# Performance work log

Measured on AMD Instinct MI355X. Metric: run time of the kernel, lower is better.

## Reference

```python
import jax, jax.numpy as jnp
import numpy as np

N = 100000      # nodes
E = 1600000     # edges (before self-loops)
IN = 128        # in_channels
H = 8           # heads (layer 0)
C = 8           # hidden_node_channels_per_head
OUT = 64        # out_channels (layer 1, single head, concat=False)
NEG_SLOPE = 0.2 # PyG GATConv LeakyReLU slope


def setup_inputs() -> dict:
    key = jax.random.key(0)
    ks = jax.random.split(key, 10)
    x = jax.random.normal(ks[0], (N, IN), jnp.float32)
    edge_index = jax.random.randint(ks[1], (2, E), 0, N, dtype=jnp.int32)
    s0 = 1.0 / np.sqrt(IN)
    s1 = 1.0 / np.sqrt(H * C)
    return {
        "x": x,
        "edge_index": edge_index,
        "W0": jax.random.normal(ks[2], (IN, H * C), jnp.float32) * s0,
        "att_src0": jax.random.normal(ks[3], (H, C), jnp.float32) * s1,
        "att_dst0": jax.random.normal(ks[4], (H, C), jnp.float32) * s1,
        "b0": jnp.zeros((H * C,), jnp.float32),
        "W1": jax.random.normal(ks[5], (H * C, OUT), jnp.float32) * s1,
        "att_src1": jax.random.normal(ks[6], (1, OUT), jnp.float32) * s1,
        "att_dst1": jax.random.normal(ks[7], (1, OUT), jnp.float32) * s1,
        "b1": jnp.zeros((OUT,), jnp.float32),
    }


def _gat_conv(x, src, dst, W, a_src, a_dst, b, heads, ch, concat):
    # x: [N, F_in]; src/dst: [E'] (self-loops included)
    xW = (x @ W).reshape(N, heads, ch)                     # [N, H, C]
    a_s = jnp.einsum('nhc,hc->nh', xW, a_src)              # [N, H]
    a_d = jnp.einsum('nhc,hc->nh', xW, a_dst)              # [N, H]
    e = jax.nn.leaky_relu(a_s[src] + a_d[dst], NEG_SLOPE)  # [E', H]
    # segment softmax over incoming edges of each dst node
    m = jax.ops.segment_max(e, dst, num_segments=N)        # [N, H]
    ex = jnp.exp(e - m[dst])
    denom = jax.ops.segment_sum(ex, dst, num_segments=N)   # [N, H]
    alpha = ex / denom[dst]                                # [E', H]
    out = jax.ops.segment_sum(alpha[:, :, None] * xW[src], dst, num_segments=N)  # [N, H, C]
    if concat:
        return out.reshape(N, heads * ch) + b
    return out.mean(axis=1) + b


def reference(x, edge_index, W0, att_src0, att_dst0, b0, W1, att_src1, att_dst1, b1):
    src, dst = edge_index[0], edge_index[1]
    loops = jnp.arange(N, dtype=src.dtype)                 # PyG add_self_loops=True
    src = jnp.concatenate([src, loops])
    dst = jnp.concatenate([dst, loops])
    # layer 0: GATConv(IN -> C per head, H heads, concat) ; ELU (dropout = identity at eval)
    h = jax.nn.elu(_gat_conv(x, src, dst, W0, att_src0, att_dst0, b0, H, C, True))
    # layer 1: GATConv(H*C -> OUT, 1 head, concat=False) ; ELU
    out = jax.nn.elu(_gat_conv(h, src, dst, W1, att_src1, att_dst1, b1, 1, OUT, False))
    return out
```

## Files before the change

### kernel.cpp

```cpp
#include <hip/hip_runtime.h>
#include <hip/hip_fp16.h>
#include <math.h>


#define CAPS 16
#define STRIDE 17
#define NBMAX 512
#define LOG2E 1.44269504f

typedef _Float16 h2_t  __attribute__((ext_vector_type(2)));
typedef _Float16 h8_t  __attribute__((ext_vector_type(8)));
typedef float    f4_t  __attribute__((ext_vector_type(4)));
typedef unsigned int u4_t __attribute__((ext_vector_type(4)));

__device__ __forceinline__ float lrelu(float v) { return v >= 0.f ? v : 0.2f * v; }
__device__ __forceinline__ float eluf(float v)  { return v > 0.f ? v : expm1f(v); }

#define MIX_LO(acc, pk, w) asm("v_fma_mix_f32 %0, %1, %2, %0 op_sel:[0,0,0] op_sel_hi:[1,0,0]" : "+v"(acc) : "v"(pk), "v"(w))
#define MIX_HI(acc, pk, w) asm("v_fma_mix_f32 %0, %1, %2, %0 op_sel:[1,0,0] op_sel_hi:[1,0,0]" : "+v"(acc) : "v"(pk), "v"(w))

__global__ void kPrep(const float* __restrict__ W0,
                      const float* __restrict__ aS0, const float* __restrict__ aD0,
                      const float* __restrict__ W1,
                      __half* __restrict__ W0swz, __half* __restrict__ W1swz)
{
    for (int g = threadIdx.x; g < 1280; g += 256) {
        int col  = g & 15;
        int quad = (g >> 4) & 3;
        int ks   = (g >> 6) & 3;
        int ct   = g >> 8;
        #pragma unroll
        for (int j = 0; j < 8; j++) {
            int k = ks * 32 + quad * 8 + j;
            float v;
            if (ct < 4) {
                v = W0[k * 64 + ct * 16 + col];
            } else {
                int h = col & 7;
                const float* att = (col < 8) ? aS0 : aD0;
                v = 0.f;
                #pragma unroll
                for (int cc = 0; cc < 8; cc++)
                    v += W0[k * 64 + h * 8 + cc] * att[h * 8 + cc];
            }
            W0swz[g * 8 + j] = __float2half(v);
        }
    }
    for (int g = threadIdx.x; g < 512; g += 256) {
        int col  = g & 15;
        int quad = (g >> 4) & 3;
        int ks   = (g >> 6) & 1;
        int ct   = g >> 7;
        #pragma unroll
        for (int j = 0; j < 8; j++) {
            int k = ks * 32 + quad * 8 + j;
            W1swz[g * 8 + j] = __float2half(W1[k * 64 + ct * 16 + col]);
        }
    }
}

__device__ __forceinline__ void gemm_body(
    int gb, const float* __restrict__ x, int N,
    __half* __restrict__ xw, float* __restrict__ as, float* __restrict__ ad,
    h8_t* Bl)
{
    int wave = threadIdx.x >> 6, lane = threadIdx.x & 63;
    int row0 = gb * 128 + wave * 16;
    if (row0 >= N) return;
    int quad = lane >> 4, c16 = lane & 15;
    int myrow = min(row0 + c16, N - 1);
    const float* xr = x + (size_t)myrow * 128;
    h8_t a[4];
    #pragma unroll
    for (int ks = 0; ks < 4; ks++) {
        int kb = ks * 32 + quad * 8;
        float4 v0 = *(const float4*)(xr + kb);
        float4 v1 = *(const float4*)(xr + kb + 4);
        h8_t av;
        av[0] = (_Float16)v0.x; av[1] = (_Float16)v0.y;
        av[2] = (_Float16)v0.z; av[3] = (_Float16)v0.w;
        av[4] = (_Float16)v1.x; av[5] = (_Float16)v1.y;
        av[6] = (_Float16)v1.z; av[7] = (_Float16)v1.w;
        a[ks] = av;
    }
    int rbase = row0 + quad * 4;
    #pragma unroll
    for (int ct = 0; ct < 5; ct++) {
        f4_t acc = {0.f, 0.f, 0.f, 0.f};
        #pragma unroll
        for (int ks = 0; ks < 4; ks++) {
            h8_t b = Bl[(ct * 4 + ks) * 64 + lane];
            acc = __builtin_amdgcn_mfma_f32_16x16x32_f16(a[ks], b, acc, 0, 0, 0);
        }
        if (ct < 4) {
            int col = ct * 16 + c16;
            #pragma unroll
            for (int r = 0; r < 4; r++) {
                int row = rbase + r;
                if (row < N) xw[(size_t)row * 64 + col] = __float2half(acc[r]);
            }
        } else {
            #pragma unroll
            for (int r = 0; r < 4; r++) {
                int row = rbase + r;
                if (row < N) {
                    float sc = acc[r] * LOG2E;
                    if (c16 < 8) as[(size_t)row * 8 + c16] = sc;
                    else         ad[(size_t)row * 8 + (c16 - 8)] = sc;
                }
            }
        }
    }
}

__global__ __launch_bounds__(512, 4) void kGB(
    const float* __restrict__ x, const __half* __restrict__ W0swz, int N,
    __half* __restrict__ xw, float* __restrict__ as, float* __restrict__ ad,
    int gemmBlocks,
    const int* __restrict__ src, const int* __restrict__ dst, int E, int perBlock,
    unsigned* __restrict__ bucketBuf, int* __restrict__ gcur, int NB, int cap,
    int binBlocks)
{
    __shared__ __align__(16) char smem[NBMAX * STRIDE * 4 + NBMAX * 4];
    int b = blockIdx.x;
    int T = gemmBlocks + binBlocks;
    int lo = (int)((long long)b * gemmBlocks / T);
    int hi = (int)((long long)(b + 1) * gemmBlocks / T);
    if (hi > lo) {
        h8_t* Bl = (h8_t*)smem;
        const float4* s = (const float4*)W0swz;
        float4* d = (float4*)smem;
        for (int i = threadIdx.x; i < 1280; i += 512) d[i] = s[i];
        __syncthreads();
        gemm_body(lo, x, N, xw, as, ad, Bl);
    } else {
        int pb = b - hi;
        unsigned* stage = (unsigned*)smem;
        int* scnt = (int*)(smem + NBMAX * STRIDE * 4);
        int tid = threadIdx.x;
        for (int i = tid; i < NB; i += 512) scnt[i] = 0;
        __syncthreads();
        int e0 = pb * perBlock, e1 = min(E, e0 + perBlock);
        for (int i = e0 + tid; i < e1; i += 512) {
            int d2 = dst[i], s2 = src[i];
            int bk = d2 >> 8;
            unsigned rec = ((unsigned)(d2 & 255) << 22) | (unsigned)s2;
            int pos = atomicAdd(&scnt[bk], 1);
            if (pos < CAPS) {
                stage[bk * STRIDE + pos] = rec;
            } else {
                int g = atomicAdd(&gcur[bk], 1);
                if (g < cap) bucketBuf[(size_t)bk * cap + g] = rec;
            }
        }
        __syncthreads();
        for (int t = tid; t < NB; t += 512) {
            int n = min(scnt[t], CAPS);
            if (n > 0) {
                int gb2 = atomicAdd(&gcur[t], n);
                unsigned* gp = &bucketBuf[(size_t)t * cap + gb2];
                for (int j = 0; j < n; j++)
                    if (gb2 + j < cap) gp[j] = stage[t * STRIDE + j];
            }
        }
    }
}

__global__ __launch_bounds__(256) void kP2(
    const unsigned* __restrict__ bucketBuf, const int* __restrict__ gcur,
    int NB, int cap, int N, int* __restrict__ row, int* __restrict__ adj)
{
    __shared__ int deg[256];
    __shared__ int curl[256];
    __shared__ int sc[256];
    int b = blockIdx.x, tid = threadIdx.x;
    int lo = b << 8;
    int hi = min(N, lo + 256);
    int cnt = hi - lo;
    int size = min(gcur[b], cap);
    int part = 0;
    for (int i = tid; i < b; i += 256) part += min(gcur[i], cap);
    sc[tid] = part;
    __syncthreads();
    for (int off = 128; off > 0; off >>= 1) {
        if (tid < off) sc[tid] += sc[tid + off];
        __syncthreads();
    }
    int bbase = sc[0];
    __syncthreads();
    deg[tid] = 0;
    __syncthreads();
    const unsigned* buf = bucketBuf + (size_t)b * cap;
    for (int e = tid; e < size; e += 256) atomicAdd(&deg[buf[e] >> 22], 1);
    __syncthreads();
    int d = deg[tid];
    sc[tid] = d;
    __syncthreads();
    for (int off = 1; off < 256; off <<= 1) {
        int xv = (tid >= off) ? sc[tid - off] : 0;
        __syncthreads();
        sc[tid] += xv;
        __syncthreads();
    }
    int o = (tid ? sc[tid - 1] : 0);
    curl[tid] = o;
    if (tid < cnt) row[lo + tid] = bbase + o;
    if (b == NB - 1 && tid == 0) row[N] = bbase + size;
    __syncthreads();
    for (int e = tid; e < size; e += 256) {
        unsigned r = buf[e];
        int l = r >> 22;
        int p = atomicAdd(&curl[l], 1);
        adj[bbase + p] = (int)(r & 0x3FFFFF);
    }
}

__global__ __launch_bounds__(256) void k_agg8(
    const __half* __restrict__ xw, const float* __restrict__ as, const float* __restrict__ ad,
    const int* __restrict__ row, const int* __restrict__ adj,
    const float* __restrict__ bias, int N, __half* __restrict__ hbuf)
{
    int n = (blockIdx.x * 256 + threadIdx.x) >> 5;
    int lane = threadIdx.x & 63;
    int sub  = lane & 31;
    if (n >= N) return;
    int e4 = sub >> 3;
    int hh = sub & 7;
    int rs = row[n], re = row[n + 1];
    const u4_t* xwv = (const u4_t*)xw;
    float adv = ad[(unsigned)n * 8u + hh];
    float shift = lrelu(as[(unsigned)n * 8u + hh] + adv);
    float accv[8];
    #pragma unroll
    for (int k = 0; k < 8; k++) accv[k] = 0.f;
    float dsum = 0.f;

    int j = rs;
    bool vA0 = j + e4 < re,      vB0 = j + 4 + e4 < re;
    int  sA0 = adj[(unsigned)(vA0 ? j + e4 : 0)];
    int  sB0 = adj[(unsigned)(vB0 ? j + 4 + e4 : 0)];
    bool vA1 = j + 8 + e4 < re,  vB1 = j + 12 + e4 < re;
    int  sA1 = adj[(unsigned)(vA1 ? j + 8 + e4 : 0)];
    int  sB1 = adj[(unsigned)(vB1 ? j + 12 + e4 : 0)];
    float eA0 = lrelu(as[(unsigned)sA0 * 8u + hh] + adv);
    float eB0 = lrelu(as[(unsigned)sB0 * 8u + hh] + adv);
    u4_t xA0 = xwv[(unsigned)sA0 * 8u + hh];
    u4_t xB0 = xwv[(unsigned)sB0 * 8u + hh];
    float eA1, eB1; u4_t xA1, xB1;

    for (;;) {
        {
            bool vA2 = j + 16 + e4 < re, vB2 = j + 20 + e4 < re;
            int nsA = adj[(unsigned)(vA2 ? j + 16 + e4 : 0)];
            int nsB = adj[(unsigned)(vB2 ? j + 20 + e4 : 0)];
            eA1 = lrelu(as[(unsigned)sA1 * 8u + hh] + adv);
            eB1 = lrelu(as[(unsigned)sB1 * 8u + hh] + adv);
            xA1 = xwv[(unsigned)sA1 * 8u + hh];
            xB1 = xwv[(unsigned)sB1 * 8u + hh];
            float wA = vA0 ? __builtin_amdgcn_exp2f(eA0 - shift) : 0.f;
            float wB = vB0 ? __builtin_amdgcn_exp2f(eB0 - shift) : 0.f;
            dsum += wA + wB;
            #pragma unroll
            for (int q = 0; q < 4; q++) {
                MIX_LO(accv[2 * q],     xA0[q], wA);
                MIX_HI(accv[2 * q + 1], xA0[q], wA);
            }
            #pragma unroll
            for (int q = 0; q < 4; q++) {
                MIX_LO(accv[2 * q],     xB0[q], wB);
                MIX_HI(accv[2 * q + 1], xB0[q], wB);
            }
            vA0 = vA2; vB0 = vB2; sA0 = nsA; sB0 = nsB;
        }
        j += 8;
        if (!__any(vA1)) break;
        {
            bool vA2 = j + 16 + e4 < re, vB2 = j + 20 + e4 < re;
            int nsA = adj[(unsigned)(vA2 ? j + 16 + e4 : 0)];
            int nsB = adj[(unsigned)(vB2 ? j + 20 + e4 : 0)];
            eA0 = lrelu(as[(unsigned)sA0 * 8u + hh] + adv);
            eB0 = lrelu(as[(unsigned)sB0 * 8u + hh] + adv);
            xA0 = xwv[(unsigned)sA0 * 8u + hh];
            xB0 = xwv[(unsigned)sB0 * 8u + hh];
            float wA = vA1 ? __builtin_amdgcn_exp2f(eA1 - shift) : 0.f;
            float wB = vB1 ? __builtin_amdgcn_exp2f(eB1 - shift) : 0.f;
            dsum += wA + wB;
            #pragma unroll
            for (int q = 0; q < 4; q++) {
                MIX_LO(accv[2 * q],     xA1[q], wA);
                MIX_HI(accv[2 * q + 1], xA1[q], wA);
            }
            #pragma unroll
            for (int q = 0; q < 4; q++) {
                MIX_LO(accv[2 * q],     xB1[q], wB);
                MIX_HI(accv[2 * q + 1], xB1[q], wB);
            }
            vA1 = vA2; vB1 = vB2; sA1 = nsA; sB1 = nsB;
        }
        j += 8;
        if (!__any(vA0)) break;
    }
    #pragma unroll
    for (int k = 0; k < 8; k++) {
        accv[k] += __shfl_xor(accv[k], 8, 64);
        accv[k] += __shfl_xor(accv[k], 16, 64);
    }
    dsum += __shfl_xor(dsum, 8, 64);
    dsum += __shfl_xor(dsum, 16, 64);
    if (e4 == 0) {
        float inv = 1.f / (1.f + dsum);
        h8_t sv = *(const h8_t*)(xw + (size_t)n * 64 + hh * 8);
        float4 b0 = *(const float4*)(bias + hh * 8);
        float4 b1 = *(const float4*)(bias + hh * 8 + 4);
        float bb[8] = {b0.x, b0.y, b0.z, b0.w, b1.x, b1.y, b1.z, b1.w};
        h8_t o;
        #pragma unroll
        for (int k = 0; k < 8; k++) {
            float v = (accv[k] + (float)sv[k]) * inv + bb[k];
            o[k] = (_Float16)eluf(v);
        }
        *(h8_t*)(hbuf + (size_t)n * 64 + hh * 8) = o;
    }
}

__global__ __launch_bounds__(512, 4) void kTF1(
    const __half* __restrict__ h, const __half* __restrict__ W1swz,
    const float* __restrict__ aS1, const float* __restrict__ aD1, int N,
    __half* __restrict__ hw, float* __restrict__ as1, float* __restrict__ ad1)
{
    __shared__ __align__(16) h8_t Bl[512];
    {
        const float4* s = (const float4*)W1swz;
        float4* d = (float4*)Bl;
        for (int i = threadIdx.x; i < 512; i += 512) d[i] = s[i];
    }
    __syncthreads();
    int wave = threadIdx.x >> 6, lane = threadIdx.x & 63;
    int row0 = blockIdx.x * 128 + wave * 16;
    if (row0 >= N) return;
    int quad = lane >> 4, c16 = lane & 15;
    int myrow = min(row0 + c16, N - 1);
    const __half* hr = h + (size_t)myrow * 64;
    h8_t a0 = *(const h8_t*)(hr + quad * 8);
    h8_t a1 = *(const h8_t*)(hr + 32 + quad * 8);
    int rbase = row0 + quad * 4;
    float ps[4] = {0.f, 0.f, 0.f, 0.f};
    float pd[4] = {0.f, 0.f, 0.f, 0.f};
    #pragma unroll
    for (int ct = 0; ct < 4; ct++) {
        f4_t acc = {0.f, 0.f, 0.f, 0.f};
        acc = __builtin_amdgcn_mfma_f32_16x16x32_f16(a0, Bl[(ct * 2 + 0) * 64 + lane], acc, 0, 0, 0);
        acc = __builtin_amdgcn_mfma_f32_16x16x32_f16(a1, Bl[(ct * 2 + 1) * 64 + lane], acc, 0, 0, 0);
        float s1c = aS1[ct * 16 + c16];
        float d1c = aD1[ct * 16 + c16];
        int col = ct * 16 + c16;
        #pragma unroll
        for (int r = 0; r < 4; r++) {
            int rr = rbase + r;
            if (rr < N) hw[(size_t)rr * 64 + col] = __float2half(acc[r]);
            ps[r] = fmaf(acc[r], s1c, ps[r]);
            pd[r] = fmaf(acc[r], d1c, pd[r]);
        }
    }
    #pragma unroll
    for (int r = 0; r < 4; r++) {
        #pragma unroll
        for (int off = 1; off < 16; off <<= 1) {
            ps[r] += __shfl_xor(ps[r], off, 64);
            pd[r] += __shfl_xor(pd[r], off, 64);
        }
    }
    if (c16 == 0) {
        #pragma unroll
        for (int r = 0; r < 4; r++) {
            int rr = rbase + r;
            if (rr < N) { as1[rr] = ps[r] * LOG2E; ad1[rr] = pd[r] * LOG2E; }
        }
    }
}

__global__ __launch_bounds__(256) void k_agg1(
    const __half* __restrict__ hw, const float* __restrict__ as, const float* __restrict__ ad,
    const int* __restrict__ row, const int* __restrict__ adj,
    const float* __restrict__ bias, int N, float* __restrict__ outp)
{
    int n = (blockIdx.x * 256 + threadIdx.x) >> 5;
    int lane = threadIdx.x & 63;
    int sub  = lane & 31;
    if (n >= N) return;
    int e4 = sub >> 3;
    int hh = sub & 7;
    int rs = row[n], re = row[n + 1];
    const u4_t* hwv = (const u4_t*)hw;
    float adv = ad[n];
    float shift = lrelu(as[n] + adv);
    float accv[8];
    #pragma unroll
    for (int k = 0; k < 8; k++) accv[k] = 0.f;
    float dsum = 0.f;

    int j = rs;
    bool vA0 = j + e4 < re,      vB0 = j + 4 + e4 < re;
    int  sA0 = adj[(unsigned)(vA0 ? j + e4 : 0)];
    int  sB0 = adj[(unsigned)(vB0 ? j + 4 + e4 : 0)];
    bool vA1 = j + 8 + e4 < re,  vB1 = j + 12 + e4 < re;
    int  sA1 = adj[(unsigned)(vA1 ? j + 8 + e4 : 0)];
    int  sB1 = adj[(unsigned)(vB1 ? j + 12 + e4 : 0)];
    float eA0 = lrelu(as[(unsigned)sA0] + adv);
    float eB0 = lrelu(as[(unsigned)sB0] + adv);
    u4_t xA0 = hwv[(unsigned)sA0 * 8u + hh];
    u4_t xB0 = hwv[(unsigned)sB0 * 8u + hh];
    float eA1, eB1; u4_t xA1, xB1;

    for (;;) {
        {
            bool vA2 = j + 16 + e4 < re, vB2 = j + 20 + e4 < re;
            int nsA = adj[(unsigned)(vA2 ? j + 16 + e4 : 0)];
            int nsB = adj[(unsigned)(vB2 ? j + 20 + e4 : 0)];
            eA1 = lrelu(as[(unsigned)sA1] + adv);
            eB1 = lrelu(as[(unsigned)sB1] + adv);
            xA1 = hwv[(unsigned)sA1 * 8u + hh];
            xB1 = hwv[(unsigned)sB1 * 8u + hh];
            float wA = vA0 ? __builtin_amdgcn_exp2f(eA0 - shift) : 0.f;
            float wB = vB0 ? __builtin_amdgcn_exp2f(eB0 - shift) : 0.f;
            dsum += wA + wB;
            #pragma unroll
            for (int q = 0; q < 4; q++) {
                MIX_LO(accv[2 * q],     xA0[q], wA);
                MIX_HI(accv[2 * q + 1], xA0[q], wA);
            }
            #pragma unroll
            for (int q = 0; q < 4; q++) {
                MIX_LO(accv[2 * q],     xB0[q], wB);
                MIX_HI(accv[2 * q + 1], xB0[q], wB);
            }
            vA0 = vA2; vB0 = vB2; sA0 = nsA; sB0 = nsB;
        }
        j += 8;
        if (!__any(vA1)) break;
        {
            bool vA2 = j + 16 + e4 < re, vB2 = j + 20 + e4 < re;
            int nsA = adj[(unsigned)(vA2 ? j + 16 + e4 : 0)];
            int nsB = adj[(unsigned)(vB2 ? j + 20 + e4 : 0)];
            eA0 = lrelu(as[(unsigned)sA0] + adv);
            eB0 = lrelu(as[(unsigned)sB0] + adv);
            xA0 = hwv[(unsigned)sA0 * 8u + hh];
            xB0 = hwv[(unsigned)sB0 * 8u + hh];
            float wA = vA1 ? __builtin_amdgcn_exp2f(eA1 - shift) : 0.f;
            float wB = vB1 ? __builtin_amdgcn_exp2f(eB1 - shift) : 0.f;
            dsum += wA + wB;
            #pragma unroll
            for (int q = 0; q < 4; q++) {
                MIX_LO(accv[2 * q],     xA1[q], wA);
                MIX_HI(accv[2 * q + 1], xA1[q], wA);
            }
            #pragma unroll
            for (int q = 0; q < 4; q++) {
                MIX_LO(accv[2 * q],     xB1[q], wB);
                MIX_HI(accv[2 * q + 1], xB1[q], wB);
            }
            vA1 = vA2; vB1 = vB2; sA1 = nsA; sB1 = nsB;
        }
        j += 8;
        if (!__any(vA0)) break;
    }
    #pragma unroll
    for (int k = 0; k < 8; k++) {
        accv[k] += __shfl_xor(accv[k], 8, 64);
        accv[k] += __shfl_xor(accv[k], 16, 64);
    }
    dsum += __shfl_xor(dsum, 8, 64);
    dsum += __shfl_xor(dsum, 16, 64);
    if (e4 == 0) {
        float inv = 1.f / (1.f + dsum);
        h8_t sv = *(const h8_t*)(hw + (size_t)n * 64 + hh * 8);
        float4 b0 = *(const float4*)(bias + hh * 8);
        float4 b1 = *(const float4*)(bias + hh * 8 + 4);
        float bb[8] = {b0.x, b0.y, b0.z, b0.w, b1.x, b1.y, b1.z, b1.w};
        float ov[8];
        #pragma unroll
        for (int k = 0; k < 8; k++)
            ov[k] = eluf((accv[k] + (float)sv[k]) * inv + bb[k]);
        float4 o0 = {ov[0], ov[1], ov[2], ov[3]};
        float4 o1 = {ov[4], ov[5], ov[6], ov[7]};
        float4* op = (float4*)(outp + (size_t)n * 64 + hh * 8);
        op[0] = o0;
        op[1] = o1;
    }
}

extern "C" void kernel_launch(void* const* d_in, const int* in_sizes, int n_in,
                              void* d_out, int out_size, void* d_ws, size_t ws_size,
                              hipStream_t stream)
{
    const float* x   = (const float*)d_in[0];
    const int*   ei  = (const int*)d_in[1];
    const float* W0  = (const float*)d_in[2];
    const float* aS0 = (const float*)d_in[3];
    const float* aD0 = (const float*)d_in[4];
    const float* b0  = (const float*)d_in[5];
    const float* W1  = (const float*)d_in[6];
    const float* aS1 = (const float*)d_in[7];
    const float* aD1 = (const float*)d_in[8];
    const float* b1  = (const float*)d_in[9];

    const int N = in_sizes[0] / 128;
    const int E = in_sizes[1] / 2;
    const int* srcp = ei;
    const int* dstp = ei + E;

    const int NB  = (N + 255) >> 8;
    const int cap = E / NB + 4096;

    char* ws = (char*)d_ws;
    size_t off = 0;
    auto alloc = [&](size_t bytes) -> size_t {
        size_t o = off;
        off = (o + bytes + 255) & ~(size_t)255;
        return o;
    };
    __half* B1 = (__half*)(ws + alloc((size_t)N * 64 * 2));
    size_t b2Bytes = (size_t)N * 64 * 2;
    size_t bkBytes = (size_t)NB * cap * 4;
    char*  region  = ws + alloc(b2Bytes > bkBytes ? b2Bytes : bkBytes);
    __half*   B2        = (__half*)region;
    unsigned* bucketBuf = (unsigned*)region;
    float* as0 = (float*)(ws + alloc((size_t)N * 8 * 4));
    float* ad0 = (float*)(ws + alloc((size_t)N * 8 * 4));
    float* as1 = (float*)(ws + alloc((size_t)N * 4));
    float* ad1 = (float*)(ws + alloc((size_t)N * 4));
    int*   row = (int*)(ws + alloc((size_t)(N + 1) * 4));
    int*   adj = (int*)(ws + alloc((size_t)E * 4));
    int*  gcur = (int*)(ws + alloc((size_t)NB * 4));
    __half* W0swz = (__half*)(ws + alloc(1280 * 8 * 2));
    __half* W1swz = (__half*)(ws + alloc(512 * 8 * 2));

    const int gemmBlocks = (N + 127) / 128;
    const int binBlocks  = 1024;
    const int perBlock   = (E + binBlocks - 1) / binBlocks;

    hipMemsetAsync(gcur, 0, (size_t)NB * 4, stream);
    kPrep<<<1, 256, 0, stream>>>(W0, aS0, aD0, W1, W0swz, W1swz);
    kGB<<<gemmBlocks + binBlocks, 512, 0, stream>>>(
        x, W0swz, N, B1, as0, ad0, gemmBlocks,
        srcp, dstp, E, perBlock, bucketBuf, gcur, NB, cap, binBlocks);
    kP2<<<NB, 256, 0, stream>>>(bucketBuf, gcur, NB, cap, N, row, adj);

    const int agBlocks = (N + 7) / 8;
    k_agg8<<<agBlocks, 256, 0, stream>>>(B1, as0, ad0, row, adj, b0, N, B2);
    kTF1<<<(N + 127) / 128, 512, 0, stream>>>(B2, W1swz, aS1, aD1, N, B1, as1, ad1);
    k_agg1<<<agBlocks, 256, 0, stream>>>(B1, as1, ad1, row, adj, b1, N, (float*)d_out);
}
```

Measured before the change: 264.8 us.

## Fold weight swizzle into consumer kernels, halve bin blocks, use fast ELU

```diff
diff --git a/kernel.cpp b/kernel.cpp
--- a/kernel.cpp
+++ b/kernel.cpp
@@ -14,50 +14,12 @@
 typedef unsigned int u4_t __attribute__((ext_vector_type(4)));
 
 __device__ __forceinline__ float lrelu(float v) { return v >= 0.f ? v : 0.2f * v; }
-__device__ __forceinline__ float eluf(float v)  { return v > 0.f ? v : expm1f(v); }
+__device__ __forceinline__ float eluf(float v)  {
+    return v > 0.f ? v : __builtin_amdgcn_exp2f(v * LOG2E) - 1.f;
+}
 
 #define MIX_LO(acc, pk, w) asm("v_fma_mix_f32 %0, %1, %2, %0 op_sel:[0,0,0] op_sel_hi:[1,0,0]" : "+v"(acc) : "v"(pk), "v"(w))
 #define MIX_HI(acc, pk, w) asm("v_fma_mix_f32 %0, %1, %2, %0 op_sel:[1,0,0] op_sel_hi:[1,0,0]" : "+v"(acc) : "v"(pk), "v"(w))
-
-__global__ void kPrep(const float* __restrict__ W0,
-                      const float* __restrict__ aS0, const float* __restrict__ aD0,
-                      const float* __restrict__ W1,
-                      __half* __restrict__ W0swz, __half* __restrict__ W1swz)
-{
-    for (int g = threadIdx.x; g < 1280; g += 256) {
-        int col  = g & 15;
-        int quad = (g >> 4) & 3;
-        int ks   = (g >> 6) & 3;
-        int ct   = g >> 8;
-        #pragma unroll
-        for (int j = 0; j < 8; j++) {
-            int k = ks * 32 + quad * 8 + j;
-            float v;
-            if (ct < 4) {
-                v = W0[k * 64 + ct * 16 + col];
-            } else {
-                int h = col & 7;
-                const float* att = (col < 8) ? aS0 : aD0;
-                v = 0.f;
-                #pragma unroll
-                for (int cc = 0; cc < 8; cc++)
-                    v += W0[k * 64 + h * 8 + cc] * att[h * 8 + cc];
-            }
-            W0swz[g * 8 + j] = __float2half(v);
-        }
-    }
-    for (int g = threadIdx.x; g < 512; g += 256) {
-        int col  = g & 15;
-        int quad = (g >> 4) & 3;
-        int ks   = (g >> 6) & 1;
-        int ct   = g >> 7;
-        #pragma unroll
-        for (int j = 0; j < 8; j++) {
-            int k = ks * 32 + quad * 8 + j;
-            W1swz[g * 8 + j] = __float2half(W1[k * 64 + ct * 16 + col]);
-        }
-    }
-}
 
 __device__ __forceinline__ void gemm_body(
     int gb, const float* __restrict__ x, int N,
@@ -114,7 +76,8 @@
 }
 
 __global__ __launch_bounds__(512, 4) void kGB(
-    const float* __restrict__ x, const __half* __restrict__ W0swz, int N,
+    const float* __restrict__ x, const float* __restrict__ W0,
+    const float* __restrict__ aS0, const float* __restrict__ aD0, int N,
     __half* __restrict__ xw, float* __restrict__ as, float* __restrict__ ad,
     int gemmBlocks,
     const int* __restrict__ src, const int* __restrict__ dst, int E, int perBlock,
@@ -128,9 +91,33 @@
     int hi = (int)((long long)(b + 1) * gemmBlocks / T);
     if (hi > lo) {
         h8_t* Bl = (h8_t*)smem;
-        const float4* s = (const float4*)W0swz;
-        float4* d = (float4*)smem;
-        for (int i = threadIdx.x; i < 1280; i += 512) d[i] = s[i];
+        for (int g = threadIdx.x; g < 1280; g += 512) {
+            int col  = g & 15;
+            int quad = (g >> 4) & 3;
+            int ks   = (g >> 6) & 3;
+            int ct   = g >> 8;
+            h8_t av;
+            if (ct < 4) {
+                #pragma unroll
+                for (int j = 0; j < 8; j++) {
+                    int k = ks * 32 + quad * 8 + j;
+                    av[j] = (_Float16)W0[k * 64 + ct * 16 + col];
+                }
+            } else {
+                int h = col & 7;
+                const float* att = (col < 8) ? aS0 : aD0;
+                #pragma unroll
+                for (int j = 0; j < 8; j++) {
+                    int k = ks * 32 + quad * 8 + j;
+                    float v = 0.f;
+                    #pragma unroll
+                    for (int cc = 0; cc < 8; cc++)
+                        v += W0[k * 64 + h * 8 + cc] * att[h * 8 + cc];
+                    av[j] = (_Float16)v;
+                }
+            }
+            Bl[g] = av;
+        }
         __syncthreads();
         gemm_body(lo, x, N, xw, as, ad, Bl);
     } else {
@@ -324,15 +311,24 @@
 }
 
 __global__ __launch_bounds__(512, 4) void kTF1(
-    const __half* __restrict__ h, const __half* __restrict__ W1swz,
+    const __half* __restrict__ h, const float* __restrict__ W1,
     const float* __restrict__ aS1, const float* __restrict__ aD1, int N,
     __half* __restrict__ hw, float* __restrict__ as1, float* __restrict__ ad1)
 {
     __shared__ __align__(16) h8_t Bl[512];
     {
-        const float4* s = (const float4*)W1swz;
-        float4* d = (float4*)Bl;
-        for (int i = threadIdx.x; i < 512; i += 512) d[i] = s[i];
+        int g = threadIdx.x;
+        int col  = g & 15;
+        int quad = (g >> 4) & 3;
+        int ks   = (g >> 6) & 1;
+        int ct   = g >> 7;
+        h8_t av;
+        #pragma unroll
+        for (int j = 0; j < 8; j++) {
+            int k = ks * 32 + quad * 8 + j;
+            av[j] = (_Float16)W1[k * 64 + ct * 16 + col];
+        }
+        Bl[g] = av;
     }
     __syncthreads();
     int wave = threadIdx.x >> 6, lane = threadIdx.x & 63;
@@ -532,22 +528,19 @@
     int*   row = (int*)(ws + alloc((size_t)(N + 1) * 4));
     int*   adj = (int*)(ws + alloc((size_t)E * 4));
     int*  gcur = (int*)(ws + alloc((size_t)NB * 4));
-    __half* W0swz = (__half*)(ws + alloc(1280 * 8 * 2));
-    __half* W1swz = (__half*)(ws + alloc(512 * 8 * 2));
 
     const int gemmBlocks = (N + 127) / 128;
-    const int binBlocks  = 1024;
+    const int binBlocks  = 512;
     const int perBlock   = (E + binBlocks - 1) / binBlocks;
 
     hipMemsetAsync(gcur, 0, (size_t)NB * 4, stream);
-    kPrep<<<1, 256, 0, stream>>>(W0, aS0, aD0, W1, W0swz, W1swz);
     kGB<<<gemmBlocks + binBlocks, 512, 0, stream>>>(
-        x, W0swz, N, B1, as0, ad0, gemmBlocks,
+        x, W0, aS0, aD0, N, B1, as0, ad0, gemmBlocks,
         srcp, dstp, E, perBlock, bucketBuf, gcur, NB, cap, binBlocks);
     kP2<<<NB, 256, 0, stream>>>(bucketBuf, gcur, NB, cap, N, row, adj);
 
     const int agBlocks = (N + 7) / 8;
     k_agg8<<<agBlocks, 256, 0, stream>>>(B1, as0, ad0, row, adj, b0, N, B2);
-    kTF1<<<(N + 127) / 128, 512, 0, stream>>>(B2, W1swz, aS1, aD1, N, B1, as1, ad1);
+    kTF1<<<(N + 127) / 128, 512, 0, stream>>>(B2, W1, aS1, aD1, N, B1, as1, ad1);
     k_agg1<<<agBlocks, 256, 0, stream>>>(B1, as1, ad1, row, adj, b1, N, (float*)d_out);
 }
```

Result: faster. 245.2 us (-7.4%).
